# Performance work log

Measured on AMD Instinct MI355X. Metric: run time of the kernel, lower is better.

The kernel has to match this reference:

```python
import jax, jax.numpy as jnp
import numpy as np

NUM_HEADS = 16

def setup_inputs() -> dict:
    key = jax.random.key(0)
    ks = jax.random.split(key, 9)
    B, S, H = 2, 2048, 1024
    sc = 0.02
    return {
        "x":  jax.random.normal(ks[0], (B, S, H), jnp.float32),
        "Wq": jax.random.normal(ks[1], (H, H), jnp.float32) * sc,
        "bq": jnp.zeros((H,), jnp.float32),
        "Wk": jax.random.normal(ks[2], (H, H), jnp.float32) * sc,
        "bk": jnp.zeros((H,), jnp.float32),
        "Wv": jax.random.normal(ks[3], (H, H), jnp.float32) * sc,
        "bv": jnp.zeros((H,), jnp.float32),
        "Wo": jax.random.normal(ks[4], (H, H), jnp.float32) * sc,
        "bo": jnp.zeros((H,), jnp.float32),
    }

def _split_heads(t, nh):
    B, S, H = t.shape
    return t.reshape(B, S, nh, H // nh).transpose(0, 2, 1, 3)  # [B, nh, S, hd]

def reference(x, Wq, bq, Wk, bk, Wv, bv, Wo, bo):
    # mask_type == 'gaussian', dropout = 0 (eval), return_weights = False
    B, S, H = x.shape
    nh = NUM_HEADS
    q = _split_heads(x @ Wq + bq, nh)  # [B, nh, S, hd]
    k = _split_heads(x @ Wk + bk, nh)
    v = _split_heads(x @ Wv + bv, nh)
    dif = q - k  # elementwise, as in the original
    # exp(-dif @ dif^T / 2)
    score = jnp.exp(-0.5 * jnp.einsum('bhqd,bhkd->bhqk', dif, dif))
    # gaussian mask: 1 strictly above the diagonal, 0 on/below (faithful to source)
    mask = jnp.triu(jnp.ones((S, S), x.dtype), k=1)
    prob = score * mask  # [B, nh, S, S]
    ctx = jnp.einsum('bhqk,bhkd->bhqd', prob, v)  # [B, nh, S, hd]
    ctx = ctx.transpose(0, 2, 1, 3).reshape(B, S, H)
    return ctx @ Wo + bo
```

## Files before the change

kernel.cpp:

```cpp
#include <hip/hip_runtime.h>
#include <math.h>

constexpr int SEQ  = 2048;
constexpr int HID  = 1024;
constexpr int MTOT = 4096;
constexpr int BH   = 32;

typedef _Float16 f16;
typedef _Float16 f16x8 __attribute__((ext_vector_type(8)));
typedef float    f32x4 __attribute__((ext_vector_type(4)));

__global__ __launch_bounds__(256) void prep(const float* __restrict__ x,
                                            const float* __restrict__ Wq,
                                            const float* __restrict__ Wk,
                                            const float* __restrict__ Wv,
                                            const float* __restrict__ Wo,
                                            f16* __restrict__ xh,
                                            f16* __restrict__ WqkT,
                                            f16* __restrict__ WvT,
                                            f16* __restrict__ WoT) {
    __shared__ f16 T[64][72];
    const int z = blockIdx.z;
    const int t = threadIdx.x;

    if (z == 3) {
        const int chunk = blockIdx.y * 16 + blockIdx.x;
        const float* src = x + (size_t)chunk * 16384;
        f16* dst = xh + (size_t)chunk * 16384;
#pragma unroll
        for (int it = 0; it < 16; it++) {
            const int i = it * 1024 + t * 4;
            float4 v = *(const float4*)(src + i);
            f16 o[4] = {(f16)v.x, (f16)v.y, (f16)v.z, (f16)v.w};
            *(ushort4*)(dst + i) = *(ushort4*)o;
        }
        return;
    }

    const float* W  = (z == 0) ? Wq : (z == 1) ? Wv : Wo;
    f16* WT = (z == 0) ? WqkT : (z == 1) ? WvT : WoT;
    const int k0 = blockIdx.x * 64, n0 = blockIdx.y * 64;
    const int r  = t >> 4;
    const int c4 = (t & 15) * 4;
#pragma unroll
    for (int rr = 0; rr < 64; rr += 16) {
        float4 w = *(const float4*)(W + (size_t)(k0 + rr + r) * HID + n0 + c4);
        if (z == 0) {
            float4 w2 = *(const float4*)(Wk + (size_t)(k0 + rr + r) * HID + n0 + c4);
            w.x -= w2.x; w.y -= w2.y; w.z -= w2.z; w.w -= w2.w;
        }
        T[c4 + 0][rr + r] = (f16)w.x;
        T[c4 + 1][rr + r] = (f16)w.y;
        T[c4 + 2][rr + r] = (f16)w.z;
        T[c4 + 3][rr + r] = (f16)w.w;
    }
    __syncthreads();
#pragma unroll
    for (int pp = 0; pp < 2; pp++) {
        const int nr = pp * 32 + (t >> 3);
        const int kc = (t & 7) * 8;
        *(uint4*)(WT + (size_t)(n0 + nr) * HID + k0 + kc) = *(uint4*)(&T[nr][kc]);
    }
}

__global__ __launch_bounds__(256) void proj_gemm(const f16* __restrict__ A,
                                                 const f16* __restrict__ WqkT,
                                                 const f16* __restrict__ WvT,
                                                 const float* __restrict__ bq,
                                                 const float* __restrict__ bk,
                                                 const float* __restrict__ bv,
                                                 f16* __restrict__ dif,
                                                 f16* __restrict__ vT) {
    __shared__ f16 As[2][128 * 72];
    __shared__ f16 Bs[2][128 * 72];
    const int t = threadIdx.x;
    const int m0  = blockIdx.x * 128;
    const int n0g = blockIdx.y * 128;
    const bool isv = (n0g >= HID);
    const f16* BT = isv ? WvT : WqkT;
    const int n0 = n0g & (HID - 1);
    const int w = t >> 6, l = t & 63, quad = l >> 4, ln = l & 15;
    const int wm = (w >> 1) * 64, wn = (w & 1) * 64;
    const int srow = t >> 1, shalf = (t & 1) * 32;

    const f16* pa = A  + (size_t)(m0 + srow) * HID + shalf;
    const f16* pb = BT + (size_t)(n0 + srow) * HID + shalf;

    uint4 ar0 = *(const uint4*)(pa),      ar1 = *(const uint4*)(pa + 8);
    uint4 ar2 = *(const uint4*)(pa + 16), ar3 = *(const uint4*)(pa + 24);
    uint4 br0 = *(const uint4*)(pb),      br1 = *(const uint4*)(pb + 8);
    uint4 br2 = *(const uint4*)(pb + 16), br3 = *(const uint4*)(pb + 24);

    f32x4 acc[4][4] = {};
    int buf = 0;

    for (int k0 = 0; k0 < HID; k0 += 64) {
        f16* da = As[buf] + srow * 72 + shalf;
        f16* db = Bs[buf] + srow * 72 + shalf;
        *(uint4*)(da)      = ar0; *(uint4*)(da + 8)  = ar1;
        *(uint4*)(da + 16) = ar2; *(uint4*)(da + 24) = ar3;
        *(uint4*)(db)      = br0; *(uint4*)(db + 8)  = br1;
        *(uint4*)(db + 16) = br2; *(uint4*)(db + 24) = br3;
        __syncthreads();
        if (k0 + 64 < HID) {
            const f16* qa = pa + k0 + 64;
            const f16* qb = pb + k0 + 64;
            ar0 = *(const uint4*)(qa);      ar1 = *(const uint4*)(qa + 8);
            ar2 = *(const uint4*)(qa + 16); ar3 = *(const uint4*)(qa + 24);
            br0 = *(const uint4*)(qb);      br1 = *(const uint4*)(qb + 8);
            br2 = *(const uint4*)(qb + 16); br3 = *(const uint4*)(qb + 24);
        }
#pragma unroll
        for (int kh = 0; kh < 2; kh++) {
            f16x8 af[4], bf[4];
#pragma unroll
            for (int mt = 0; mt < 4; mt++)
                af[mt] = *(const f16x8*)(As[buf] + (wm + mt * 16 + ln) * 72 + kh * 32 + quad * 8);
#pragma unroll
            for (int nt = 0; nt < 4; nt++)
                bf[nt] = *(const f16x8*)(Bs[buf] + (wn + nt * 16 + ln) * 72 + kh * 32 + quad * 8);
#pragma unroll
            for (int mt = 0; mt < 4; mt++)
#pragma unroll
                for (int nt = 0; nt < 4; nt++)
                    acc[mt][nt] = __builtin_amdgcn_mfma_f32_16x16x32_f16(
                        af[mt], bf[nt], acc[mt][nt], 0, 0, 0);
        }
        buf ^= 1;
    }

#pragma unroll
    for (int mt = 0; mt < 4; mt++) {
#pragma unroll
        for (int nt = 0; nt < 4; nt++) {
            const int nl = n0 + wn + nt * 16 + ln;
            const int m_base = m0 + wm + mt * 16 + quad * 4;
            const int h = nl >> 6, e = nl & 63;
            if (!isv) {
                const float bb = bq[nl] - bk[nl];
#pragma unroll
                for (int r = 0; r < 4; r++) {
                    const int m = m_base + r;
                    const int b = m >> 11, s = m & 2047;
                    dif[((size_t)(b * 16 + h) * SEQ + s) * 64 + e] =
                        (f16)(acc[mt][nt][r] + bb);
                }
            } else {
                const float bb = bv[nl];
                const int b = m_base >> 11, s0 = m_base & 2047;
                f16 o[4];
#pragma unroll
                for (int r = 0; r < 4; r++) o[r] = (f16)(acc[mt][nt][r] + bb);
                *(ushort4*)(&vT[((size_t)(b * 16 + h) * 64 + e) * SEQ + s0]) =
                    *(ushort4*)o;
            }
        }
    }
}

__global__ __launch_bounds__(256) void out_gemm(const f16* __restrict__ C0,
                                                const f16* __restrict__ C1,
                                                const f16* __restrict__ WoT,
                                                const float* __restrict__ bo,
                                                float* __restrict__ out) {
    __shared__ f16 As[2][128 * 72];
    __shared__ f16 Bs[2][64 * 72];
    const int t = threadIdx.x;
    const int m0 = blockIdx.x * 128, n0 = blockIdx.y * 64;
    const int w = t >> 6, l = t & 63, quad = l >> 4, ln = l & 15;
    const int wm = (w >> 1) * 64, wn = (w & 1) * 32;
    const int arow = t >> 1, ahalf = (t & 1) * 32;
    const int brow = t >> 2, boff = (t & 3) * 16;

    const f16* pa0 = C0  + (size_t)(m0 + arow) * HID + ahalf;
    const f16* pa1 = C1  + (size_t)(m0 + arow) * HID + ahalf;
    const f16* pb  = WoT + (size_t)(n0 + brow) * HID + boff;

    f16x8 a0 = *(const f16x8*)(pa0)      + *(const f16x8*)(pa1);
    f16x8 a1 = *(const f16x8*)(pa0 + 8)  + *(const f16x8*)(pa1 + 8);
    f16x8 a2 = *(const f16x8*)(pa0 + 16) + *(const f16x8*)(pa1 + 16);
    f16x8 a3 = *(const f16x8*)(pa0 + 24) + *(const f16x8*)(pa1 + 24);
    uint4 b0 = *(const uint4*)(pb), b1 = *(const uint4*)(pb + 8);

    f32x4 acc[4][2] = {};
    int buf = 0;

    for (int k0 = 0; k0 < HID; k0 += 64) {
        f16* da = As[buf] + arow * 72 + ahalf;
        *(f16x8*)(da)      = a0; *(f16x8*)(da + 8)  = a1;
        *(f16x8*)(da + 16) = a2; *(f16x8*)(da + 24) = a3;
        f16* db = Bs[buf] + brow * 72 + boff;
        *(uint4*)(db) = b0; *(uint4*)(db + 8) = b1;
        __syncthreads();
        if (k0 + 64 < HID) {
            const int kn = k0 + 64;
            a0 = *(const f16x8*)(pa0 + kn)      + *(const f16x8*)(pa1 + kn);
            a1 = *(const f16x8*)(pa0 + kn + 8)  + *(const f16x8*)(pa1 + kn + 8);
            a2 = *(const f16x8*)(pa0 + kn + 16) + *(const f16x8*)(pa1 + kn + 16);
            a3 = *(const f16x8*)(pa0 + kn + 24) + *(const f16x8*)(pa1 + kn + 24);
            b0 = *(const uint4*)(pb + kn); b1 = *(const uint4*)(pb + kn + 8);
        }
#pragma unroll
        for (int kh = 0; kh < 2; kh++) {
            f16x8 af[4], bf[2];
#pragma unroll
            for (int mt = 0; mt < 4; mt++)
                af[mt] = *(const f16x8*)(As[buf] + (wm + mt * 16 + ln) * 72 + kh * 32 + quad * 8);
#pragma unroll
            for (int nt = 0; nt < 2; nt++)
                bf[nt] = *(const f16x8*)(Bs[buf] + (wn + nt * 16 + ln) * 72 + kh * 32 + quad * 8);
#pragma unroll
            for (int mt = 0; mt < 4; mt++)
#pragma unroll
                for (int nt = 0; nt < 2; nt++)
                    acc[mt][nt] = __builtin_amdgcn_mfma_f32_16x16x32_f16(
                        af[mt], bf[nt], acc[mt][nt], 0, 0, 0);
        }
        buf ^= 1;
    }

#pragma unroll
    for (int mt = 0; mt < 4; mt++)
#pragma unroll
        for (int nt = 0; nt < 2; nt++) {
            const int n = n0 + wn + nt * 16 + ln;
            const float bb = bo[n];
            const int m_base = m0 + wm + mt * 16 + quad * 4;
#pragma unroll
            for (int r = 0; r < 4; r++)
                out[(size_t)(m_base + r) * HID + n] =
                    acc[mt][nt][r] * 65536.0f + bb;
        }
}

__global__ __launch_bounds__(256) void attn_f16(const f16* __restrict__ dif,
                                                const f16* __restrict__ vT,
                                                f16* __restrict__ ctx0,
                                                f16* __restrict__ ctx1) {
    __shared__ f16 Qs[64 * 72];
    __shared__ f16 Ks[64 * 72];
    __shared__ f16 Vs[64 * 72];
    __shared__ f16 Ps[64 * 72];

    const int pq = blockIdx.x, bh = blockIdx.y, ks = blockIdx.z;
    f16* Cout = ks ? ctx1 : ctx0;
    const f16* D  = dif + (size_t)bh * SEQ * 64;
    const f16* VT = vT  + (size_t)bh * 64 * SEQ;
    const int b = bh >> 4, h = bh & 15;
    const int t = threadIdx.x, w = t >> 6, l = t & 63, quad = l >> 4, ln = l & 15;
    const int ve = t >> 2, vc = (t & 3) * 16;

    for (int half = 0; half < 2; half++) {
        const int qt = half ? (31 - pq) : pq;
        const int i0 = qt * 64;
        __syncthreads();

#pragma unroll
        for (int rr = 0; rr < 2; rr++) {
            const int o = rr * 2048 + t * 8;
            uint4 v = *(const uint4*)(D + i0 * 64 + o);
            *(uint4*)(Qs + (o >> 6) * 72 + (o & 63)) = v;
        }

        f32x4 acc[4] = {};
        const int kt0 = qt + ks;

        uint4 kr0, kr1, vr0, vr1;
        if (kt0 < 32) {
            const int j0 = kt0 * 64;
            kr0 = *(const uint4*)(D + j0 * 64 + t * 8);
            kr1 = *(const uint4*)(D + j0 * 64 + 2048 + t * 8);
            vr0 = *(const uint4*)(VT + (size_t)ve * SEQ + j0 + vc);
            vr1 = *(const uint4*)(VT + (size_t)ve * SEQ + j0 + vc + 8);
        }

        for (int kt = kt0; kt < 32; kt += 2) {
            __syncthreads();

            {
                const int o0 = t * 8, o1 = 2048 + t * 8;
                *(uint4*)(Ks + (o0 >> 6) * 72 + (o0 & 63)) = kr0;
                *(uint4*)(Ks + (o1 >> 6) * 72 + (o1 & 63)) = kr1;
                *(uint4*)(Vs + ve * 72 + vc)     = vr0;
                *(uint4*)(Vs + ve * 72 + vc + 8) = vr1;
            }
            __syncthreads();

            if (kt + 2 < 32) {
                const int j2 = (kt + 2) * 64;
                kr0 = *(const uint4*)(D + j2 * 64 + t * 8);
                kr1 = *(const uint4*)(D + j2 * 64 + 2048 + t * 8);
                vr0 = *(const uint4*)(VT + (size_t)ve * SEQ + j2 + vc);
                vr1 = *(const uint4*)(VT + (size_t)ve * SEQ + j2 + vc + 8);
            }

            f32x4 s[4] = {};
#pragma unroll
            for (int kh = 0; kh < 2; kh++) {
                f16x8 a = *(const f16x8*)(Qs + (w * 16 + ln) * 72 + kh * 32 + quad * 8);
#pragma unroll
                for (int nt = 0; nt < 4; nt++) {
                    f16x8 bfr = *(const f16x8*)(Ks + (nt * 16 + ln) * 72 + kh * 32 + quad * 8);
                    s[nt] = __builtin_amdgcn_mfma_f32_16x16x32_f16(a, bfr, s[nt], 0, 0, 0);
                }
            }

            const bool full = (kt > qt);
#pragma unroll
            for (int nt = 0; nt < 4; nt++)
#pragma unroll
                for (int r = 0; r < 4; r++) {
                    const int iloc = w * 16 + quad * 4 + r;
                    const int jloc = nt * 16 + ln;
                    float p = (full || (jloc > iloc))
                                  ? fminf(__expf(-0.5f * s[nt][r]) * 0x1p-16f, 60000.0f)
                                  : 0.0f;
                    Ps[iloc * 72 + jloc] = (f16)p;
                }

#pragma unroll
            for (int kh = 0; kh < 2; kh++) {
                f16x8 a = *(const f16x8*)(Ps + (w * 16 + ln) * 72 + kh * 32 + quad * 8);
#pragma unroll
                for (int nt = 0; nt < 4; nt++) {
                    f16x8 bfr = *(const f16x8*)(Vs + (nt * 16 + ln) * 72 + kh * 32 + quad * 8);
                    acc[nt] = __builtin_amdgcn_mfma_f32_16x16x32_f16(a, bfr, acc[nt], 0, 0, 0);
                }
            }
        }

#pragma unroll
        for (int nt = 0; nt < 4; nt++)
#pragma unroll
            for (int r = 0; r < 4; r++) {
                const int iloc = w * 16 + quad * 4 + r;
                Cout[(size_t)(b * SEQ + i0 + iloc) * HID + h * 64 + nt * 16 + ln] =
                    (f16)acc[nt][r];
            }
    }
}

extern "C" void kernel_launch(void* const* d_in, const int* in_sizes, int n_in,
                              void* d_out, int out_size, void* d_ws, size_t ws_size,
                              hipStream_t stream) {
    const float* x  = (const float*)d_in[0];
    const float* Wq = (const float*)d_in[1];
    const float* bq = (const float*)d_in[2];
    const float* Wk = (const float*)d_in[3];
    const float* bk = (const float*)d_in[4];
    const float* Wv = (const float*)d_in[5];
    const float* bv = (const float*)d_in[6];
    const float* Wo = (const float*)d_in[7];
    const float* bo = (const float*)d_in[8];
    float* out = (float*)d_out;

    char* ws = (char*)d_ws;
    f16* xh   = (f16*)(ws);
    f16* WqkT = (f16*)(ws + (8 << 20));
    f16* WvT  = (f16*)(ws + (10 << 20));
    f16* WoT  = (f16*)(ws + (12 << 20));
    f16* dif  = (f16*)(ws + (14 << 20));
    f16* vT   = (f16*)(ws + (22 << 20));
    f16* ctx0 = (f16*)(ws + (30 << 20));
    f16* ctx1 = (f16*)(ws + (38 << 20));

    prep<<<dim3(16, 16, 4), 256, 0, stream>>>(x, Wq, Wk, Wv, Wo,
                                              xh, WqkT, WvT, WoT);
    proj_gemm<<<dim3(MTOT / 128, 16), 256, 0, stream>>>(xh, WqkT, WvT,
                                                        bq, bk, bv, dif, vT);
    attn_f16<<<dim3(16, BH, 2), 256, 0, stream>>>(dif, vT, ctx0, ctx1);
    out_gemm<<<dim3(MTOT / 128, 16), 256, 0, stream>>>(ctx0, ctx1, WoT, bo, out);
}
```

Measured before the change: 188.0 us.

## Shrink projection GEMM tiles, hoist Q fragments, fold exp scaling into FMA

The projection GEMM moves from 128x128 to 128x64 tiles with a single LDS buffer and a launch bound of 4 blocks per CU. This doubles the grid and is meant to raise occupancy and balance the work across CUs, at the cost of less operand reuse per block. The attention kernel now loads its Q fragments into registers once per query tile instead of on every key tile, and adds a barrier before that load. The 2^-16 scale is folded into the exponent as an additive constant inside an fmaf, which removes one multiply per score element.

```diff
diff --git a/kernel.cpp b/kernel.cpp
--- a/kernel.cpp
+++ b/kernel.cpp
@@ -63,44 +63,43 @@
     }
 }
 
-__global__ __launch_bounds__(256) void proj_gemm(const f16* __restrict__ A,
-                                                 const f16* __restrict__ WqkT,
-                                                 const f16* __restrict__ WvT,
-                                                 const float* __restrict__ bq,
-                                                 const float* __restrict__ bk,
-                                                 const float* __restrict__ bv,
-                                                 f16* __restrict__ dif,
-                                                 f16* __restrict__ vT) {
-    __shared__ f16 As[2][128 * 72];
-    __shared__ f16 Bs[2][128 * 72];
+__global__ __launch_bounds__(256, 4) void proj_gemm(const f16* __restrict__ A,
+                                                    const f16* __restrict__ WqkT,
+                                                    const f16* __restrict__ WvT,
+                                                    const float* __restrict__ bq,
+                                                    const float* __restrict__ bk,
+                                                    const float* __restrict__ bv,
+                                                    f16* __restrict__ dif,
+                                                    f16* __restrict__ vT) {
+    __shared__ f16 As[128 * 72];
+    __shared__ f16 Bs[64 * 72];
     const int t = threadIdx.x;
     const int m0  = blockIdx.x * 128;
-    const int n0g = blockIdx.y * 128;
+    const int n0g = blockIdx.y * 64;
     const bool isv = (n0g >= HID);
     const f16* BT = isv ? WvT : WqkT;
     const int n0 = n0g & (HID - 1);
     const int w = t >> 6, l = t & 63, quad = l >> 4, ln = l & 15;
-    const int wm = (w >> 1) * 64, wn = (w & 1) * 64;
-    const int srow = t >> 1, shalf = (t & 1) * 32;
-
-    const f16* pa = A  + (size_t)(m0 + srow) * HID + shalf;
-    const f16* pb = BT + (size_t)(n0 + srow) * HID + shalf;
+    const int wm = w * 32;
+    const int arow = t >> 1, ahalf = (t & 1) * 32;
+    const int brow = t >> 2, boff = (t & 3) * 16;
+
+    const f16* pa = A  + (size_t)(m0 + arow) * HID + ahalf;
+    const f16* pb = BT + (size_t)(n0 + brow) * HID + boff;
 
     uint4 ar0 = *(const uint4*)(pa),      ar1 = *(const uint4*)(pa + 8);
     uint4 ar2 = *(const uint4*)(pa + 16), ar3 = *(const uint4*)(pa + 24);
     uint4 br0 = *(const uint4*)(pb),      br1 = *(const uint4*)(pb + 8);
-    uint4 br2 = *(const uint4*)(pb + 16), br3 = *(const uint4*)(pb + 24);
-
-    f32x4 acc[4][4] = {};
-    int buf = 0;
+
+    f32x4 acc[2][4] = {};
 
     for (int k0 = 0; k0 < HID; k0 += 64) {
-        f16* da = As[buf] + srow * 72 + shalf;
-        f16* db = Bs[buf] + srow * 72 + shalf;
+        __syncthreads();
+        f16* da = As + arow * 72 + ahalf;
         *(uint4*)(da)      = ar0; *(uint4*)(da + 8)  = ar1;
         *(uint4*)(da + 16) = ar2; *(uint4*)(da + 24) = ar3;
-        *(uint4*)(db)      = br0; *(uint4*)(db + 8)  = br1;
-        *(uint4*)(db + 16) = br2; *(uint4*)(db + 24) = br3;
+        f16* db = Bs + brow * 72 + boff;
+        *(uint4*)(db) = br0; *(uint4*)(db + 8) = br1;
         __syncthreads();
         if (k0 + 64 < HID) {
             const f16* qa = pa + k0 + 64;
@@ -108,32 +107,30 @@
             ar0 = *(const uint4*)(qa);      ar1 = *(const uint4*)(qa + 8);
             ar2 = *(const uint4*)(qa + 16); ar3 = *(const uint4*)(qa + 24);
             br0 = *(const uint4*)(qb);      br1 = *(const uint4*)(qb + 8);
-            br2 = *(const uint4*)(qb + 16); br3 = *(const uint4*)(qb + 24);
         }
 #pragma unroll
         for (int kh = 0; kh < 2; kh++) {
-            f16x8 af[4], bf[4];
-#pragma unroll
-            for (int mt = 0; mt < 4; mt++)
-                af[mt] = *(const f16x8*)(As[buf] + (wm + mt * 16 + ln) * 72 + kh * 32 + quad * 8);
+            f16x8 af[2], bf[4];
+#pragma unroll
+            for (int mt = 0; mt < 2; mt++)
+                af[mt] = *(const f16x8*)(As + (wm + mt * 16 + ln) * 72 + kh * 32 + quad * 8);
 #pragma unroll
             for (int nt = 0; nt < 4; nt++)
-                bf[nt] = *(const f16x8*)(Bs[buf] + (wn + nt * 16 + ln) * 72 + kh * 32 + quad * 8);
-#pragma unroll
-            for (int mt = 0; mt < 4; mt++)
+                bf[nt] = *(const f16x8*)(Bs + (nt * 16 + ln) * 72 + kh * 32 + quad * 8);
+#pragma unroll
+            for (int mt = 0; mt < 2; mt++)
 #pragma unroll
                 for (int nt = 0; nt < 4; nt++)
                     acc[mt][nt] = __builtin_amdgcn_mfma_f32_16x16x32_f16(
                         af[mt], bf[nt], acc[mt][nt], 0, 0, 0);
         }
-        buf ^= 1;
-    }
-
-#pragma unroll
-    for (int mt = 0; mt < 4; mt++) {
+    }
+
+#pragma unroll
+    for (int mt = 0; mt < 2; mt++) {
 #pragma unroll
         for (int nt = 0; nt < 4; nt++) {
-            const int nl = n0 + wn + nt * 16 + ln;
+            const int nl = n0 + nt * 16 + ln;
             const int m_base = m0 + wm + mt * 16 + quad * 4;
             const int h = nl >> 6, e = nl & 63;
             if (!isv) {
@@ -261,6 +258,11 @@
             uint4 v = *(const uint4*)(D + i0 * 64 + o);
             *(uint4*)(Qs + (o >> 6) * 72 + (o & 63)) = v;
         }
+        __syncthreads();
+        f16x8 aq[2];
+#pragma unroll
+        for (int kh = 0; kh < 2; kh++)
+            aq[kh] = *(const f16x8*)(Qs + (w * 16 + ln) * 72 + kh * 32 + quad * 8);
 
         f32x4 acc[4] = {};
         const int kt0 = qt + ks;
@@ -296,14 +298,12 @@
 
             f32x4 s[4] = {};
 #pragma unroll
-            for (int kh = 0; kh < 2; kh++) {
-                f16x8 a = *(const f16x8*)(Qs + (w * 16 + ln) * 72 + kh * 32 + quad * 8);
+            for (int kh = 0; kh < 2; kh++)
 #pragma unroll
                 for (int nt = 0; nt < 4; nt++) {
                     f16x8 bfr = *(const f16x8*)(Ks + (nt * 16 + ln) * 72 + kh * 32 + quad * 8);
-                    s[nt] = __builtin_amdgcn_mfma_f32_16x16x32_f16(a, bfr, s[nt], 0, 0, 0);
+                    s[nt] = __builtin_amdgcn_mfma_f32_16x16x32_f16(aq[kh], bfr, s[nt], 0, 0, 0);
                 }
-            }
 
             const bool full = (kt > qt);
 #pragma unroll
@@ -313,7 +313,8 @@
                     const int iloc = w * 16 + quad * 4 + r;
                     const int jloc = nt * 16 + ln;
                     float p = (full || (jloc > iloc))
-                                  ? fminf(__expf(-0.5f * s[nt][r]) * 0x1p-16f, 60000.0f)
+                                  ? fminf(__expf(fmaf(s[nt][r], -0.5f,
+                                                      -11.090354888959125f)), 60000.0f)
                                   : 0.0f;
                     Ps[iloc * 72 + jloc] = (f16)p;
                 }
@@ -366,7 +367,7 @@
 
     prep<<<dim3(16, 16, 4), 256, 0, stream>>>(x, Wq, Wk, Wv, Wo,
                                               xh, WqkT, WvT, WoT);
-    proj_gemm<<<dim3(MTOT / 128, 16), 256, 0, stream>>>(xh, WqkT, WvT,
+    proj_gemm<<<dim3(MTOT / 128, 32), 256, 0, stream>>>(xh, WqkT, WvT,
                                                         bq, bk, bv, dif, vT);
     attn_f16<<<dim3(16, BH, 2), 256, 0, stream>>>(dif, vT, ctx0, ctx1);
     out_gemm<<<dim3(MTOT / 128, 16), 256, 0, stream>>>(ctx0, ctx1, WoT, bo, out);
```

After: 190.8 us. No clear change (+1.5%).
